# Kernel tuning notes

Measured on AMD Instinct MI355X. Metric: run time of the kernel, lower is better.

The kernel has to match this reference:

```python
import jax, jax.numpy as jnp
import numpy as np

B, NX, NY, E, H, L = 4, 1024, 1024, 512, 8, 4
DH = E // H
FF = 4 * E
SCALE = DH ** (-0.5)
EPS = 1e-5


def _ln(x, g, b):
    mu = jnp.mean(x, axis=-1, keepdims=True)
    var = jnp.mean((x - mu) ** 2, axis=-1, keepdims=True)
    return (x - mu) * jax.lax.rsqrt(var + EPS) * g + b


def setup_inputs() -> dict:
    key = jax.random.key(0)
    ks = jax.random.split(key, 16)
    s = 0.02
    inp = {
        'x': jax.random.normal(ks[0], (B, NX, E), jnp.float32),
        'y': jax.random.normal(ks[1], (B, NY, E), jnp.float32),
        'x_mask': jax.random.randint(ks[2], (B, NX), 0, 2, jnp.int32),
        'y_mask': jax.random.randint(ks[3], (B, NY), 0, 2, jnp.int32),
        # stacked per-layer params (L leading dim)
        'Wq': jax.random.normal(ks[4], (L, E, E), jnp.float32) * s,
        'bq': jnp.zeros((L, E), jnp.float32),
        'Wk': jax.random.normal(ks[5], (L, E, E), jnp.float32) * s,
        'bk': jnp.zeros((L, E), jnp.float32),
        'Wv': jax.random.normal(ks[6], (L, E, E), jnp.float32) * s,
        'bv': jnp.zeros((L, E), jnp.float32),
        'Wo': jax.random.normal(ks[7], (L, E, E), jnp.float32) * s,
        'bo': jnp.zeros((L, E), jnp.float32),
        'g1': jnp.ones((L, E), jnp.float32),
        'be1': jnp.zeros((L, E), jnp.float32),
        'g2': jnp.ones((L, E), jnp.float32),
        'be2': jnp.zeros((L, E), jnp.float32),
        'W1': jax.random.normal(ks[8], (L, E, FF), jnp.float32) * s,
        'bf1': jnp.zeros((L, FF), jnp.float32),
        'W2': jax.random.normal(ks[9], (L, FF, E), jnp.float32) * s,
        'bf2': jnp.zeros((L, E), jnp.float32),
    }
    return inp


def _forward(x, y, mask4, Wq, bq, Wk, bk, Wv, bv, Wo, bo, g1, be1, g2, be2, W1, bf1, W2, bf2):
    # mask4: (B,1,NX,NY) int, 0 = masked
    attn_prev = None
    out = x
    for l in range(L):
        q = x @ Wq[l] + bq[l]              # (B,NX,E)
        k = y @ Wk[l] + bk[l]
        v = y @ Wv[l] + bv[l]
        # faithful non-standard head split: plain reshape, no transpose
        q = q.reshape(B, H, NX, DH)
        k = k.reshape(B, H, NY, DH)
        v = v.reshape(B, H, NY, DH)
        scores = jnp.einsum('bhnd,bhmd->bhnm', q, k) * SCALE
        scores = jnp.where(mask4 == 0, jnp.float32(-1e9), scores)
        a = jax.nn.softmax(scores, axis=-1)
        if attn_prev is not None:
            a = a + attn_prev  # residual attention
        attn_prev = a
        o = jnp.einsum('bhnm,bhmd->bhnd', a, v)
        o = jnp.transpose(o, (0, 2, 1, 3)).reshape(B, NX, E)
        o = o @ Wo[l] + bo[l]
        h = _ln(x + o, g1[l], be1[l])
        ff = jax.nn.gelu(h @ W1[l] + bf1[l], approximate=False) @ W2[l] + bf2[l]
        out = _ln(h + ff, g2[l], be2[l])
        # NOTE: faithful to source, x and y are NOT updated between layers;
        # only the attention residual chains. Final output is last layer's out.
    return out


def reference(x, y, x_mask, y_mask, Wq, bq, Wk, bk, Wv, bv, Wo, bo, g1, be1, g2, be2, W1, bf1, W2, bf2):
    mask4 = (x_mask[:, :, None].astype(jnp.float32) @ y_mask[:, None, :].astype(jnp.float32)).astype(jnp.int32)[:, None]
    return _forward(x, y, mask4, Wq, bq, Wk, bk, Wv, bv, Wo, bo, g1, be1, g2, be2, W1, bf1, W2, bf2)
```

## Files before the change

kernel.cpp:

```cpp
#include <hip/hip_runtime.h>
#include <cstdint>

using u16    = unsigned short;
using u32    = unsigned int;
using bf16x8 = __attribute__((ext_vector_type(8))) __bf16;
using f32x4  = __attribute__((ext_vector_type(4))) float;

__device__ __forceinline__ u16 f2bf(float f) {
    u32 u = __builtin_bit_cast(u32, f);
    u += 0x7FFFu + ((u >> 16) & 1u);
    return (u16)(u >> 16);
}
__device__ __forceinline__ float bf2f(u16 u) {
    return __builtin_bit_cast(float, (u32)u << 16);
}
__device__ __forceinline__ u32 pk_bf16(float a, float b) {
    u32 r;
    asm("v_cvt_pk_bf16_f32 %0, %1, %2" : "=v"(r) : "v"(a), "v"(b));
    return r;
}
__device__ __forceinline__ void load_lds16(const u16* g, u16* l) {
    __builtin_amdgcn_global_load_lds((const __attribute__((address_space(1))) void*)g,
                                     (__attribute__((address_space(3))) void*)l, 16, 0, 0);
}

__global__ __launch_bounds__(256) void cvt_kernel(const float* __restrict__ in,
                                                  u16* __restrict__ out, int n)
{
    int i = (blockIdx.x * 256 + threadIdx.x) * 4;
    if (i >= n) return;
    float4 v = *(const float4*)(in + i);
    uint2 o;
    o.x = (u32)f2bf(v.x) | ((u32)f2bf(v.y) << 16);
    o.y = (u32)f2bf(v.z) | ((u32)f2bf(v.w) << 16);
    *(uint2*)(out + i) = o;
}

__global__ __launch_bounds__(256) void wtrans_kernel(const float* __restrict__ Wq,
                                                     const float* __restrict__ Wk,
                                                     const float* __restrict__ Wv,
                                                     const float* __restrict__ Wo,
                                                     const float* __restrict__ W1,
                                                     const float* __restrict__ W2,
                                                     u16* __restrict__ wt)
{
    const int gid = blockIdx.x;
    const float* src; u16* dst; int K = 512, N = 512; int n0, k0;
    if (gid < 2560) {
        int z = gid >> 8, tid = gid & 255;
        switch (z) {
            case 0: case 1: case 2: case 3:
                src = Wq + (size_t)z * 262144;        dst = wt + (size_t)z * 262144;            break;
            case 4: case 5: case 6: case 7:
                src = Wk + (size_t)(z - 4) * 262144;  dst = wt + 1048576 + (size_t)(z - 4) * 262144; break;
            case 8: src = Wv + 3 * 262144;  dst = wt + 2097152; break;
            default: src = Wo + 3 * 262144; dst = wt + 2359296; break;
        }
        n0 = (tid & 15) * 32; k0 = (tid >> 4) * 32;
    } else if (gid < 3584) {
        int tid = gid - 2560;
        src = W1 + 3 * 1048576; dst = wt + 2621440; K = 512; N = 2048;
        n0 = (tid & 63) * 32; k0 = (tid >> 6) * 32;
    } else {
        int tid = gid - 3584;
        src = W2 + 3 * 1048576; dst = wt + 3670016; K = 2048; N = 512;
        n0 = (tid & 15) * 32; k0 = (tid >> 4) * 32;
    }
    __shared__ float tile[32][33];
    int tx = threadIdx.x, ty = threadIdx.y;
    #pragma unroll
    for (int i = 0; i < 4; i++) {
        int r = ty + i * 8;
        tile[r][tx] = src[(size_t)(k0 + r) * N + n0 + tx];
    }
    __syncthreads();
    #pragma unroll
    for (int i = 0; i < 4; i++) {
        int rn = ty + i * 8;
        dst[(size_t)(n0 + rn) * K + k0 + tx] = f2bf(tile[tx][rn]);
    }
}

template<int BNF>
__device__ __forceinline__ void gemm_core32(const u16* __restrict__ A,
                                            const u16* __restrict__ BT,
                                            int K, int m0, int n0,
                                            u16 (*As)[32], u16 (*Bs)[32],
                                            f32x4 acc[4][BNF])
{
    const int t    = threadIdx.x;
    const int lane = t & 63, wid = t >> 6;
    const int wm = wid >> 1, wn = wid & 1;
    const int lrow = lane & 15, kg = lane >> 4;
    const int sr = lane >> 2;
    const int sg = ((lane & 3) ^ ((lane >> 3) & 3)) * 8;

    auto stage = [&](int buf, int ks) {
        #pragma unroll
        for (int i = 0; i < 2; i++) {
            int row = wid * 32 + i * 16;
            load_lds16(&A[(size_t)(m0 + row + sr) * K + ks + sg], &As[buf * 128 + row][0]);
        }
        if constexpr (BNF == 4) {
            #pragma unroll
            for (int i = 0; i < 2; i++) {
                int row = wid * 32 + i * 16;
                load_lds16(&BT[(size_t)(n0 + row + sr) * K + ks + sg], &Bs[buf * 128 + row][0]);
            }
        } else {
            int row = wid * 16;
            load_lds16(&BT[(size_t)(n0 + row + sr) * K + ks + sg], &Bs[buf * 64 + row][0]);
        }
    };

    stage(0, 0);
    __syncthreads();
    int buf = 0;
    for (int ks = 0; ks < K; ks += 32) {
        if (ks + 32 < K) stage(buf ^ 1, ks + 32);
        const int rg = (kg ^ ((lrow >> 1) & 3)) * 8;
        bf16x8 af[4], bfv[BNF];
        #pragma unroll
        for (int i = 0; i < 4; i++)
            af[i] = *(const bf16x8*)&As[buf * 128 + wm * 64 + i * 16 + lrow][rg];
        #pragma unroll
        for (int j = 0; j < BNF; j++)
            bfv[j] = *(const bf16x8*)&Bs[buf * (BNF * 32) + wn * (BNF * 16) + j * 16 + lrow][rg];
        #pragma unroll
        for (int i = 0; i < 4; i++)
            #pragma unroll
            for (int j = 0; j < BNF; j++)
                acc[i][j] = __builtin_amdgcn_mfma_f32_16x16x32_bf16(af[i], bfv[j], acc[i][j], 0, 0, 0);
        __syncthreads();
        buf ^= 1;
    }
}

__global__ __launch_bounds__(256) void qkv_gemm_kernel(const u16* __restrict__ x16,
                                                       const u16* __restrict__ y16,
                                                       const u16* __restrict__ wt,
                                                       u16* __restrict__ qkv,
                                                       const float* __restrict__ bq,
                                                       const float* __restrict__ bk,
                                                       const float* __restrict__ bv,
                                                       const int* __restrict__ x_mask)
{
    __shared__ u16 As[256][32];
    __shared__ u16 Bs[256][32];
    const int z = blockIdx.z;
    const u16* A; const u16* BT; const float* bias;
    if (z < 4)      { A = x16; BT = wt + (size_t)z * 262144;                 bias = bq + z * 512; }
    else if (z < 8) { A = y16; BT = wt + 1048576 + (size_t)(z - 4) * 262144; bias = bk + (z - 4) * 512; }
    else            { A = y16; BT = wt + 2097152;                            bias = bv + 3 * 512; }
    u16* out = qkv + (size_t)z * 2097152;

    const int m0 = blockIdx.y * 128, n0 = blockIdx.x * 128;
    f32x4 acc[4][4];
    #pragma unroll
    for (int i = 0; i < 4; i++)
        #pragma unroll
        for (int j = 0; j < 4; j++) acc[i][j] = f32x4{0.f, 0.f, 0.f, 0.f};
    gemm_core32<4>(A, BT, 512, m0, n0, As, Bs, acc);

    const int lane = threadIdx.x & 63, wid = threadIdx.x >> 6;
    const int wm = wid >> 1, wn = wid & 1;
    const int lrow = lane & 15, kg = lane >> 4;
    #pragma unroll
    for (int i = 0; i < 4; i++)
        #pragma unroll
        for (int j = 0; j < 4; j++)
            #pragma unroll
            for (int r = 0; r < 4; r++) {
                int row = m0 + wm * 64 + i * 16 + kg * 4 + r;
                int col = n0 + wn * 64 + j * 16 + lrow;
                float v = acc[i][j][r] + bias[col];
                if (z < 4) v *= 0.125f * (x_mask[row] ? 1.f : 0.f);
                out[(size_t)row * 512 + col] = f2bf(v);
            }
}

template<int BNF, int EPI>
__global__ __launch_bounds__(256) void gemm_bt_kernel(const u16* __restrict__ A,
                                                      const u16* __restrict__ BT,
                                                      const float* __restrict__ bias,
                                                      void* __restrict__ outp,
                                                      const float* __restrict__ res,
                                                      int N, int K)
{
    __shared__ u16 As[256][32];
    __shared__ u16 Bs[BNF * 64][32];
    const int m0 = blockIdx.y * 128, n0 = blockIdx.x * (BNF * 32);
    f32x4 acc[4][BNF];
    #pragma unroll
    for (int i = 0; i < 4; i++)
        #pragma unroll
        for (int j = 0; j < BNF; j++) acc[i][j] = f32x4{0.f, 0.f, 0.f, 0.f};
    gemm_core32<BNF>(A, BT, K, m0, n0, As, Bs, acc);

    const int lane = threadIdx.x & 63, wid = threadIdx.x >> 6;
    const int wm = wid >> 1, wn = wid & 1;
    const int lrow = lane & 15, kg = lane >> 4;
    #pragma unroll
    for (int i = 0; i < 4; i++)
        #pragma unroll
        for (int j = 0; j < BNF; j++)
            #pragma unroll
            for (int r = 0; r < 4; r++) {
                int row = m0 + wm * 64 + i * 16 + kg * 4 + r;
                int col = n0 + wn * (BNF * 16) + j * 16 + lrow;
                float v = acc[i][j][r] + bias[col];
                if constexpr (EPI == 1) {
                    ((float*)outp)[(size_t)row * N + col] = v + res[(size_t)row * N + col];
                } else {
                    v = 0.5f * v * (1.f + erff(v * 0.70710678118654752f));
                    ((u16*)outp)[(size_t)row * N + col] = f2bf(v);
                }
            }
}

__global__ __launch_bounds__(256) void vtrans_kernel(const u16* __restrict__ v, u16* __restrict__ vt)
{
    const int bh = blockIdx.y, m0 = blockIdx.x * 64;
    const int b = bh >> 3, h = bh & 7;
    const u16* src = v + (size_t)b * 524288 + (size_t)h * 65536;
    u16* dst = vt + (size_t)bh * 65536;
    __shared__ u16 tile[64][72];
    const int t = threadIdx.x;
    #pragma unroll
    for (int i = 0; i < 2; i++) {
        int idx = t + i * 256, r = idx >> 3, q = idx & 7;
        *(uint4*)&tile[r][q * 8] = *(const uint4*)&src[(size_t)(m0 + r) * 64 + q * 8];
    }
    __syncthreads();
    #pragma unroll
    for (int i = 0; i < 2; i++) {
        int idx = t + i * 256, d = idx >> 3, q = idx & 7;
        alignas(16) u16 tmp[8];
        #pragma unroll
        for (int j = 0; j < 8; j++) tmp[j] = tile[q * 8 + j][d];
        *(uint4*)&dst[(size_t)d * 1024 + m0 + q * 8] = *(uint4*)tmp;
    }
}

__global__ __launch_bounds__(256, 2) void attn_kernel(const u16* __restrict__ qkv,
                                                      const int* __restrict__ x_mask,
                                                      const int* __restrict__ y_mask,
                                                      const u16* __restrict__ vt,
                                                      u16* __restrict__ obuf)
{
    __shared__ __align__(16) char smem[45056];
    u16 (*Kb)[4][32][64] = reinterpret_cast<u16(*)[4][32][64]>(smem);
    u16 (*Vb)[64][32]    = reinterpret_cast<u16(*)[64][32]>(smem + 32768);
    float* ymb           = reinterpret_cast<float*>(smem + 40960);
    u16 (*Osh)[64][72]   = reinterpret_cast<u16(*)[64][72]>(smem);

    const int t = threadIdx.x;
    const int wid = t >> 6, lane = t & 63;
    const int lrow = lane & 15, kg = lane >> 4;

    const int gid  = blockIdx.x;
    const int orig = (gid & 7) * 64 + (gid >> 3);
    const int bh = orig >> 4, qt = orig & 15;
    const int b = bh >> 3, h = bh & 7;
    const int q0 = qt * 64;

    const size_t headoff = (size_t)b * 524288 + (size_t)h * 65536;
    const u16* Q  = qkv + (size_t)wid * 2097152 + headoff;
    const u16* VT = vt + (size_t)bh * 65536;

    for (int i = t; i < 1024; i += 256)
        ymb[i] = y_mask[b * 1024 + i] ? 0.f : -1e9f;

    const int ksrow = wid * 8 + (lane >> 3);
    const int kscol = ((lane & 7) ^ (lane >> 3)) * 8;
    const int vsrow = wid * 16 + (lane >> 2);
    const int vscol = (((lane & 3) ^ ((vsrow & 3) ^ ((vsrow >> 2) & 3))) * 8);
    const int fswz  = (lrow & 3) ^ ((lrow >> 2) & 3);

    auto stage = [&](int buf, int mt) {
        const int m0 = mt * 32;
        #pragma unroll
        for (int it = 0; it < 4; it++) {
            const u16* src = qkv + (size_t)(4 + it) * 2097152 + headoff
                           + (size_t)(m0 + ksrow) * 64 + kscol;
            load_lds16(src, &Kb[buf][it][wid * 8][0]);
        }
        load_lds16(&VT[(size_t)vsrow * 1024 + m0 + vscol], &Vb[buf][wid * 16][0]);
    };

    bf16x8 aq[4][2];
    #pragma unroll
    for (int i = 0; i < 4; i++) {
        aq[i][0] = *(const bf16x8*)&Q[(size_t)(q0 + i * 16 + lrow) * 64 + kg * 8];
        aq[i][1] = *(const bf16x8*)&Q[(size_t)(q0 + i * 16 + lrow) * 64 + 32 + kg * 8];
    }
    float xmf[4];
    #pragma unroll
    for (int i = 0; i < 4; i++) xmf[i] = x_mask[b * 1024 + q0 + i * 16 + lrow] ? 1.f : 0.f;

    const int srcA = (((2 * kg) & 3) << 4) | lrow;
    const int srcB = (((2 * kg + 1) & 3) << 4) | lrow;

    f32x4 oacc[4][4];
    float psum[4] = {0.f, 0.f, 0.f, 0.f};
    #pragma unroll
    for (int i = 0; i < 4; i++)
        #pragma unroll
        for (int d = 0; d < 4; d++) oacc[i][d] = f32x4{0.f, 0.f, 0.f, 0.f};

    stage(0, 0);
    __syncthreads();

    for (int mt = 0; mt < 32; mt++) {
        const int buf = mt & 1;
        const int m0 = mt * 32;
        if (mt < 31) stage(buf ^ 1, mt + 1);

        bf16x8 kb[2][2];
        #pragma unroll
        for (int nf = 0; nf < 2; nf++)
            #pragma unroll
            for (int kk = 0; kk < 2; kk++)
                kb[nf][kk] = *(const bf16x8*)&Kb[buf][wid][nf * 16 + lrow][((kk * 4 + kg) ^ (lrow & 7)) * 8];

        float yb[2][4];
        #pragma unroll
        for (int nf = 0; nf < 2; nf++)
            #pragma unroll
            for (int r = 0; r < 4; r++) yb[nf][r] = ymb[m0 + nf * 16 + kg * 4 + r];

        bf16x8 pa[4];
        #pragma unroll
        for (int i = 0; i < 4; i++) {
            f32x4 s0 = f32x4{0.f, 0.f, 0.f, 0.f}, s1 = f32x4{0.f, 0.f, 0.f, 0.f};
            s0 = __builtin_amdgcn_mfma_f32_16x16x32_bf16(kb[0][0], aq[i][0], s0, 0, 0, 0);
            s0 = __builtin_amdgcn_mfma_f32_16x16x32_bf16(kb[0][1], aq[i][1], s0, 0, 0, 0);
            s1 = __builtin_amdgcn_mfma_f32_16x16x32_bf16(kb[1][0], aq[i][0], s1, 0, 0, 0);
            s1 = __builtin_amdgcn_mfma_f32_16x16x32_bf16(kb[1][1], aq[i][1], s1, 0, 0, 0);
            float p0 = __expf(fmaf(xmf[i], yb[0][0], s0[0]));
            float p1 = __expf(fmaf(xmf[i], yb[0][1], s0[1]));
            float p2 = __expf(fmaf(xmf[i], yb[0][2], s0[2]));
            float p3 = __expf(fmaf(xmf[i], yb[0][3], s0[3]));
            float p4 = __expf(fmaf(xmf[i], yb[1][0], s1[0]));
            float p5 = __expf(fmaf(xmf[i], yb[1][1], s1[1]));
            float p6 = __expf(fmaf(xmf[i], yb[1][2], s1[2]));
            float p7 = __expf(fmaf(xmf[i], yb[1][3], s1[3]));
            psum[i] += ((p0 + p1) + (p2 + p3)) + ((p4 + p5) + (p6 + p7));
            u32 w0 = pk_bf16(p0, p1), w1 = pk_bf16(p2, p3);
            u32 w2 = pk_bf16(p4, p5), w3 = pk_bf16(p6, p7);
            u32 a0 = __shfl(w0, srcA), a1 = __shfl(w1, srcA);
            u32 a2 = __shfl(w0, srcB), a3 = __shfl(w1, srcB);
            u32 b0 = __shfl(w2, srcA), b1 = __shfl(w3, srcA);
            u32 b2 = __shfl(w2, srcB), b3 = __shfl(w3, srcB);
            const bool hi = (kg & 2) != 0;
            uint4 pw;
            pw.x = hi ? b0 : a0;
            pw.y = hi ? b1 : a1;
            pw.z = hi ? b2 : a2;
            pw.w = hi ? b3 : a3;
            pa[i] = __builtin_bit_cast(bf16x8, pw);
        }

        bf16x8 vbf[4];
        #pragma unroll
        for (int d = 0; d < 4; d++)
            vbf[d] = *(const bf16x8*)&Vb[buf][d * 16 + lrow][(kg ^ fswz) * 8];
        #pragma unroll
        for (int i = 0; i < 4; i++)
            #pragma unroll
            for (int d = 0; d < 4; d++)
                oacc[i][d] = __builtin_amdgcn_mfma_f32_16x16x32_bf16(pa[i], vbf[d], oacc[i][d], 0, 0, 0);

        __syncthreads();
    }

    #pragma unroll
    for (int i = 0; i < 4; i++) {
        psum[i] += __shfl_xor(psum[i], 16);
        psum[i] += __shfl_xor(psum[i], 32);
    }
    float invr[4][4];
    #pragma unroll
    for (int i = 0; i < 4; i++) {
        float inv = 1.f / psum[i];
        #pragma unroll
        for (int r = 0; r < 4; r++) invr[i][r] = __shfl(inv, kg * 4 + r, 16);
    }

    #pragma unroll
    for (int i = 0; i < 4; i++)
        #pragma unroll
        for (int d = 0; d < 4; d++)
            #pragma unroll
            for (int r = 0; r < 4; r++)
                Osh[wid][i * 16 + kg * 4 + r][d * 16 + lrow] = f2bf(oacc[i][d][r] * invr[i][r]);
    __syncthreads();

    {
        const int row = t >> 2, cbase = (t & 3) * 16;
        #pragma unroll
        for (int half = 0; half < 2; half++) {
            const int c0 = cbase + half * 8;
            float a8[8] = {0, 0, 0, 0, 0, 0, 0, 0};
            #pragma unroll
            for (int l = 0; l < 4; l++) {
                uint4 v = *(const uint4*)&Osh[l][row][c0];
                const u16* pv = (const u16*)&v;
                #pragma unroll
                for (int j = 0; j < 8; j++) a8[j] += bf2f(pv[j]);
            }
            alignas(16) u16 tmp[8];
            #pragma unroll
            for (int j = 0; j < 8; j++) tmp[j] = f2bf(a8[j]);
            *(uint4*)&obuf[(size_t)(b * 1024 + q0 + row) * 512 + h * 64 + c0] = *(uint4*)tmp;
        }
    }
}

template<int MODE>
__global__ __launch_bounds__(256) void ln_kernel(const float* __restrict__ in,
                                                 const float* __restrict__ g,
                                                 const float* __restrict__ be,
                                                 float* __restrict__ out32,
                                                 u16* __restrict__ out16)
{
    const int wid = threadIdx.x >> 6, lane = threadIdx.x & 63;
    const int row = blockIdx.x * 4 + wid;
    const float* x = in + (size_t)row * 512;
    float4 v1 = *(const float4*)&x[lane * 8];
    float4 v2 = *(const float4*)&x[lane * 8 + 4];
    float xv[8] = { v1.x, v1.y, v1.z, v1.w, v2.x, v2.y, v2.z, v2.w };
    float s = 0.f, s2 = 0.f;
    #pragma unroll
    for (int j = 0; j < 8; j++) { s += xv[j]; s2 += xv[j] * xv[j]; }
    #pragma unroll
    for (int off = 32; off > 0; off >>= 1) {
        s  += __shfl_xor(s, off, 64);
        s2 += __shfl_xor(s2, off, 64);
    }
    const float mean = s * (1.f / 512.f);
    const float var  = s2 * (1.f / 512.f) - mean * mean;
    const float rstd = rsqrtf(var + 1e-5f);
    float ov[8];
    #pragma unroll
    for (int j = 0; j < 8; j++) {
        int col = lane * 8 + j;
        ov[j] = (xv[j] - mean) * rstd * g[col] + be[col];
    }
    *(float4*)&out32[(size_t)row * 512 + lane * 8]     = float4{ ov[0], ov[1], ov[2], ov[3] };
    *(float4*)&out32[(size_t)row * 512 + lane * 8 + 4] = float4{ ov[4], ov[5], ov[6], ov[7] };
    if constexpr (MODE == 0) {
        alignas(16) u16 tmp[8];
        #pragma unroll
        for (int j = 0; j < 8; j++) tmp[j] = f2bf(ov[j]);
        *(uint4*)&out16[(size_t)row * 512 + lane * 8] = *(uint4*)tmp;
    }
}

extern "C" void kernel_launch(void* const* d_in, const int* in_sizes, int n_in,
                              void* d_out, int out_size, void* d_ws, size_t ws_size,
                              hipStream_t stream) {
    const float* x      = (const float*)d_in[0];
    const float* y      = (const float*)d_in[1];
    const int*   x_mask = (const int*)d_in[2];
    const int*   y_mask = (const int*)d_in[3];
    const float* Wq  = (const float*)d_in[4];
    const float* bq  = (const float*)d_in[5];
    const float* Wk  = (const float*)d_in[6];
    const float* bk  = (const float*)d_in[7];
    const float* Wv  = (const float*)d_in[8];
    const float* bv  = (const float*)d_in[9];
    const float* Wo  = (const float*)d_in[10];
    const float* bo  = (const float*)d_in[11];
    const float* g1  = (const float*)d_in[12];
    const float* be1 = (const float*)d_in[13];
    const float* g2  = (const float*)d_in[14];
    const float* be2 = (const float*)d_in[15];
    const float* W1  = (const float*)d_in[16];
    const float* bf1 = (const float*)d_in[17];
    const float* W2  = (const float*)d_in[18];
    const float* bf2 = (const float*)d_in[19];

    char* p = (char*)d_ws;
    auto alloc = [&](size_t bytes) { char* r = p; p += (bytes + 255) & ~(size_t)255; return r; };
    u16*   x16   = (u16*)alloc(2097152ULL * 2);
    u16*   y16   = (u16*)alloc(2097152ULL * 2);
    u16*   wt    = (u16*)alloc(4718592ULL * 2);
    u16*   qkv   = (u16*)alloc(9ULL * 2097152 * 2);
    u16*   vt    = (u16*)alloc(2097152ULL * 2);
    u16*   obuf  = (u16*)alloc(2097152ULL * 2);
    float* xo    = (float*)alloc(2097152ULL * 4);
    float* h32   = (float*)alloc(2097152ULL * 4);
    u16*   h16   = (u16*)alloc(2097152ULL * 2);
    u16*   ffmid = (u16*)alloc(8388608ULL * 2);
    float* ffout = (float*)alloc(2097152ULL * 4);
    if ((size_t)(p - (char*)d_ws) > ws_size) return;

    cvt_kernel<<<2048, 256, 0, stream>>>(x, x16, 2097152);
    cvt_kernel<<<2048, 256, 0, stream>>>(y, y16, 2097152);
    wtrans_kernel<<<4608, dim3(32, 8), 0, stream>>>(Wq, Wk, Wv, Wo, W1, W2, wt);
    qkv_gemm_kernel<<<dim3(4, 32, 9), 256, 0, stream>>>(x16, y16, wt, qkv, bq, bk, bv, x_mask);
    vtrans_kernel<<<dim3(16, 32), 256, 0, stream>>>(qkv + 8ULL * 2097152, vt);
    attn_kernel<<<512, 256, 0, stream>>>(qkv, x_mask, y_mask, vt, obuf);
    gemm_bt_kernel<2, 1><<<dim3(8, 32), 256, 0, stream>>>(obuf, wt + 2359296, bo + 3 * 512, xo, x, 512, 512);
    ln_kernel<0><<<1024, 256, 0, stream>>>(xo, g1 + 3 * 512, be1 + 3 * 512, h32, h16);
    gemm_bt_kernel<4, 2><<<dim3(16, 32), 256, 0, stream>>>(h16, wt + 2621440, bf1 + 3 * 2048, ffmid, nullptr, 2048, 512);
    gemm_bt_kernel<2, 1><<<dim3(8, 32), 256, 0, stream>>>(ffmid, wt + 3670016, bf2 + 3 * 512, ffout, h32, 512, 2048);
    ln_kernel<1><<<1024, 256, 0, stream>>>(ffout, g2 + 3 * 512, be2 + 3 * 512, (float*)d_out, nullptr);
}
```

Before: 190.2 us.

## Fold log2e into Q scale, use exp2, vectorize mask loads, merge cvt launches

Q is now pre-scaled by SCALE*log2(e), so the attention softmax can use exp2f in place of __expf and save a multiply per exponent. The y-mask reads become two float4 loads instead of scalar loads, and the PV MFMA block is wrapped in s_setprio to favour matrix issue. The two fp32->bf16 conversion launches are merged into one kernel, saving a launch. The mask bias is applied inside the exp2 argument, so it is effectively rescaled; with -1e9-style values this is harmless.

```diff
diff --git a/kernel.cpp b/kernel.cpp
--- a/kernel.cpp
+++ b/kernel.cpp
@@ -24,11 +24,15 @@
                                      (__attribute__((address_space(3))) void*)l, 16, 0, 0);
 }
 
-__global__ __launch_bounds__(256) void cvt_kernel(const float* __restrict__ in,
-                                                  u16* __restrict__ out, int n)
-{
-    int i = (blockIdx.x * 256 + threadIdx.x) * 4;
-    if (i >= n) return;
+__global__ __launch_bounds__(256) void cvt2_kernel(const float* __restrict__ a,
+                                                   const float* __restrict__ b,
+                                                   u16* __restrict__ oa,
+                                                   u16* __restrict__ ob)
+{
+    const int bid = blockIdx.x;
+    const float* in = bid < 2048 ? a : b;
+    u16* out = bid < 2048 ? oa : ob;
+    int i = ((bid & 2047) * 256 + threadIdx.x) * 4;
     float4 v = *(const float4*)(in + i);
     uint2 o;
     o.x = (u32)f2bf(v.x) | ((u32)f2bf(v.y) << 16);
@@ -174,7 +178,7 @@
                 int row = m0 + wm * 64 + i * 16 + kg * 4 + r;
                 int col = n0 + wn * 64 + j * 16 + lrow;
                 float v = acc[i][j][r] + bias[col];
-                if (z < 4) v *= 0.125f * (x_mask[row] ? 1.f : 0.f);
+                if (z < 4) v *= 0.180336880f * (x_mask[row] ? 1.f : 0.f);
                 out[(size_t)row * 512 + col] = f2bf(v);
             }
 }
@@ -323,11 +327,8 @@
             for (int kk = 0; kk < 2; kk++)
                 kb[nf][kk] = *(const bf16x8*)&Kb[buf][wid][nf * 16 + lrow][((kk * 4 + kg) ^ (lrow & 7)) * 8];
 
-        float yb[2][4];
-        #pragma unroll
-        for (int nf = 0; nf < 2; nf++)
-            #pragma unroll
-            for (int r = 0; r < 4; r++) yb[nf][r] = ymb[m0 + nf * 16 + kg * 4 + r];
+        float4 y0 = *(const float4*)&ymb[m0 + kg * 4];
+        float4 y1 = *(const float4*)&ymb[m0 + 16 + kg * 4];
 
         bf16x8 pa[4];
         #pragma unroll
@@ -337,14 +338,14 @@
             s0 = __builtin_amdgcn_mfma_f32_16x16x32_bf16(kb[0][1], aq[i][1], s0, 0, 0, 0);
             s1 = __builtin_amdgcn_mfma_f32_16x16x32_bf16(kb[1][0], aq[i][0], s1, 0, 0, 0);
             s1 = __builtin_amdgcn_mfma_f32_16x16x32_bf16(kb[1][1], aq[i][1], s1, 0, 0, 0);
-            float p0 = __expf(fmaf(xmf[i], yb[0][0], s0[0]));
-            float p1 = __expf(fmaf(xmf[i], yb[0][1], s0[1]));
-            float p2 = __expf(fmaf(xmf[i], yb[0][2], s0[2]));
-            float p3 = __expf(fmaf(xmf[i], yb[0][3], s0[3]));
-            float p4 = __expf(fmaf(xmf[i], yb[1][0], s1[0]));
-            float p5 = __expf(fmaf(xmf[i], yb[1][1], s1[1]));
-            float p6 = __expf(fmaf(xmf[i], yb[1][2], s1[2]));
-            float p7 = __expf(fmaf(xmf[i], yb[1][3], s1[3]));
+            float p0 = exp2f(fmaf(xmf[i], y0.x, s0[0]));
+            float p1 = exp2f(fmaf(xmf[i], y0.y, s0[1]));
+            float p2 = exp2f(fmaf(xmf[i], y0.z, s0[2]));
+            float p3 = exp2f(fmaf(xmf[i], y0.w, s0[3]));
+            float p4 = exp2f(fmaf(xmf[i], y1.x, s1[0]));
+            float p5 = exp2f(fmaf(xmf[i], y1.y, s1[1]));
+            float p6 = exp2f(fmaf(xmf[i], y1.z, s1[2]));
+            float p7 = exp2f(fmaf(xmf[i], y1.w, s1[3]));
             psum[i] += ((p0 + p1) + (p2 + p3)) + ((p4 + p5) + (p6 + p7));
             u32 w0 = pk_bf16(p0, p1), w1 = pk_bf16(p2, p3);
             u32 w2 = pk_bf16(p4, p5), w3 = pk_bf16(p6, p7);
@@ -365,11 +366,13 @@
         #pragma unroll
         for (int d = 0; d < 4; d++)
             vbf[d] = *(const bf16x8*)&Vb[buf][d * 16 + lrow][(kg ^ fswz) * 8];
+        __builtin_amdgcn_s_setprio(1);
         #pragma unroll
         for (int i = 0; i < 4; i++)
             #pragma unroll
             for (int d = 0; d < 4; d++)
                 oacc[i][d] = __builtin_amdgcn_mfma_f32_16x16x32_bf16(pa[i], vbf[d], oacc[i][d], 0, 0, 0);
+        __builtin_amdgcn_s_setprio(0);
 
         __syncthreads();
     }
@@ -496,8 +499,7 @@
     float* ffout = (float*)alloc(2097152ULL * 4);
     if ((size_t)(p - (char*)d_ws) > ws_size) return;
 
-    cvt_kernel<<<2048, 256, 0, stream>>>(x, x16, 2097152);
-    cvt_kernel<<<2048, 256, 0, stream>>>(y, y16, 2097152);
+    cvt2_kernel<<<4096, 256, 0, stream>>>(x, y, x16, y16);
     wtrans_kernel<<<4608, dim3(32, 8), 0, stream>>>(Wq, Wk, Wv, Wo, W1, W2, wt);
     qkv_gemm_kernel<<<dim3(4, 32, 9), 256, 0, stream>>>(x16, y16, wt, qkv, bq, bk, bv, x_mask);
     vtrans_kernel<<<dim3(16, 32), 256, 0, stream>>>(qkv + 8ULL * 2097152, vt);
```

Result: slower. 202.4 us (+6.4%).
